# Performance work log

Measured on AMD Instinct MI355X. Metric: run time of the kernel, lower is better.

The kernel has to match this reference:

```python
import jax, jax.numpy as jnp
import numpy as np

B, S, D, H = 2, 2048, 2048, 16
HD = D // H
EPS = 1e-5


def layernorm(x, scale, shift):
    mean = jnp.mean(x, axis=-1, keepdims=True)
    var = jnp.mean((x - mean) ** 2, axis=-1, keepdims=True)  # unbiased=False
    return scale * (x - mean) / jnp.sqrt(var + EPS) + shift


def gelu_buggy(x):
    # Faithful to source: tanh is applied ONLY to the constant sqrt(2/pi)
    c = jnp.tanh(jnp.sqrt(jnp.asarray(2.0 / jnp.pi, dtype=x.dtype)))
    return 0.5 * x * (1.0 + c * (x + 0.044715 * x ** 3))


def setup_inputs() -> dict:
    key = jax.random.key(0)
    ks = jax.random.split(key, 10)
    sd = 0.02
    return {
        "x": jax.random.normal(ks[0], (B, S, D), dtype=jnp.float32),
        "wq": jax.random.normal(ks[1], (D, D), dtype=jnp.float32) * sd,
        "wk": jax.random.normal(ks[2], (D, D), dtype=jnp.float32) * sd,
        "wv": jax.random.normal(ks[3], (D, D), dtype=jnp.float32) * sd,
        "wo": jax.random.normal(ks[4], (D, D), dtype=jnp.float32) * sd,
        "bo": jnp.zeros((D,), dtype=jnp.float32),
        "w1": jax.random.normal(ks[5], (D, 4 * D), dtype=jnp.float32) * sd,
        "b1": jnp.zeros((4 * D,), dtype=jnp.float32),
        "w2": jax.random.normal(ks[6], (4 * D, D), dtype=jnp.float32) * sd,
        "b2": jnp.zeros((D,), dtype=jnp.float32),
        "ln_scale": jnp.ones((D,), dtype=jnp.float32),
        "ln_shift": jnp.zeros((D,), dtype=jnp.float32),
    }


def attention(h, wq, wk, wv, wo, bo):
    b, s, _ = h.shape
    q = (h @ wq).reshape(b, s, H, HD).transpose(0, 2, 1, 3)  # [b,h,s,hd]
    k = (h @ wk).reshape(b, s, H, HD).transpose(0, 2, 1, 3)
    v = (h @ wv).reshape(b, s, H, HD).transpose(0, 2, 1, 3)
    scores = jnp.einsum('bhqd,bhkd->bhqk', q, k)
    causal = jnp.tril(jnp.ones((s, s), dtype=bool))
    scores = jnp.where(causal, scores, -jnp.inf)
    w = jax.nn.softmax(scores / jnp.sqrt(jnp.asarray(HD, dtype=h.dtype)), axis=-1)
    ctx = jnp.einsum('bhqk,bhkd->bhqd', w, v).transpose(0, 2, 1, 3).reshape(b, s, D)
    return ctx @ wo + bo


def reference(x, wq, wk, wv, wo, bo, w1, b1, w2, b2, ln_scale, ln_shift):
    # NB: source applies ln1 before BOTH sub-blocks (ln2 unused); dropout is identity (p=0 / eval)
    shortcut = x
    h = layernorm(x, ln_scale, ln_shift)
    h = attention(h, wq, wk, wv, wo, bo)
    x = h + shortcut
    shortcut = x
    h = layernorm(x, ln_scale, ln_shift)
    h = gelu_buggy(h @ w1 + b1) @ w2 + b2
    return h + shortcut
```

## Files before the change

### kernel.cpp

```cpp
#include <hip/hip_runtime.h>
#include <hip/hip_bf16.h>
#include <math.h>


typedef short bf16x8 __attribute__((ext_vector_type(8)));
typedef float f32x4 __attribute__((ext_vector_type(4)));
typedef short short4v __attribute__((ext_vector_type(4)));

#define MFMA16x32(a, b, c) __builtin_amdgcn_mfma_f32_16x16x32_bf16((a), (b), (c), 0, 0, 0)

__device__ __forceinline__ short f2bs(float f) {
    unsigned u = __builtin_bit_cast(unsigned, f);
    unsigned r = (u + 0x7FFFu + ((u >> 16) & 1u)) >> 16;
    return (short)(unsigned short)r;
}

__device__ __forceinline__ void gload_lds16(const void* g, void* l) {
    __builtin_amdgcn_global_load_lds(
        (const __attribute__((address_space(1))) unsigned int*)g,
        (__attribute__((address_space(3))) unsigned int*)l, 16, 0, 0);
}

template <int N>
__device__ __forceinline__ void vmw() {
    if constexpr (N == 0) asm volatile("s_waitcnt vmcnt(0)" ::: "memory");
    else if constexpr (N == 6) asm volatile("s_waitcnt vmcnt(6)" ::: "memory");
    else if constexpr (N == 8) asm volatile("s_waitcnt vmcnt(8)" ::: "memory");
    else if constexpr (N == 12) asm volatile("s_waitcnt vmcnt(12)" ::: "memory");
}

__global__ __launch_bounds__(256) void transpose_kernel(const float* __restrict__ in,
                                                        short* __restrict__ out,
                                                        int R, int C) {
    __shared__ float tile[32][33];
    const int tx = threadIdx.x & 31;
    const int ty = threadIdx.x >> 5;
    const int c0 = blockIdx.x * 32;
    const int r0 = blockIdx.y * 32;
#pragma unroll
    for (int i = 0; i < 4; ++i) {
        int r = ty + i * 8;
        tile[r][tx] = in[(size_t)(r0 + r) * C + c0 + tx];
    }
    __syncthreads();
#pragma unroll
    for (int i = 0; i < 4; ++i) {
        int r = ty + i * 8;
        out[(size_t)(c0 + r) * R + r0 + tx] = f2bs(tile[tx][r]);
    }
}

__global__ __launch_bounds__(256) void ln_kernel(const float* __restrict__ x,
                                                 const float* __restrict__ sc,
                                                 const float* __restrict__ sh,
                                                 short* __restrict__ out) {
    const int D = 2048;
    const int row = blockIdx.x;
    const int tid = threadIdx.x;
    __shared__ float red[4];
    const float4* xr = (const float4*)(x + (size_t)row * D);
    float4 v0 = xr[tid];
    float4 v1 = xr[tid + 256];
    float vals0[4] = {v0.x, v0.y, v0.z, v0.w};
    float vals1[4] = {v1.x, v1.y, v1.z, v1.w};

    float s = vals0[0] + vals0[1] + vals0[2] + vals0[3] + vals1[0] + vals1[1] + vals1[2] + vals1[3];
#pragma unroll
    for (int off = 32; off; off >>= 1) s += __shfl_xor(s, off);
    if ((tid & 63) == 0) red[tid >> 6] = s;
    __syncthreads();
    float mean = (red[0] + red[1] + red[2] + red[3]) * (1.0f / 2048.0f);
    __syncthreads();

    float q = 0.0f;
#pragma unroll
    for (int j = 0; j < 4; ++j) {
        float t0 = vals0[j] - mean;
        float t1 = vals1[j] - mean;
        q += t0 * t0 + t1 * t1;
    }
#pragma unroll
    for (int off = 32; off; off >>= 1) q += __shfl_xor(q, off);
    if ((tid & 63) == 0) red[tid >> 6] = q;
    __syncthreads();
    float var = (red[0] + red[1] + red[2] + red[3]) * (1.0f / 2048.0f);
    float inv = rsqrtf(var + 1e-5f);

    const int c0 = tid * 4;
    const int c1 = (tid + 256) * 4;
    short4v o0, o1;
#pragma unroll
    for (int j = 0; j < 4; ++j) {
        o0[j] = f2bs(sc[c0 + j] * ((vals0[j] - mean) * inv) + sh[c0 + j]);
        o1[j] = f2bs(sc[c1 + j] * ((vals1[j] - mean) * inv) + sh[c1 + j]);
    }
    *(short4v*)(out + (size_t)row * D + c0) = o0;
    *(short4v*)(out + (size_t)row * D + c1) = o1;
}

template <int EPI>
__global__ __launch_bounds__(512, 2) void gemm256(const short* __restrict__ Aop,
                                                  const short* __restrict__ Bt,
                                                  int M, int N, int K,
                                                  void* __restrict__ Cout,
                                                  const float* __restrict__ bias,
                                                  const float* __restrict__ res,
                                                  float gconst) {
    constexpr int TSZ = 256 * 64;
    extern __shared__ __align__(16) short lds[];
    const int tid = threadIdx.x;
    const int lane = tid & 63;
    const int wid = tid >> 6;
    const int wm = wid >> 2, wn = wid & 3;
    const int l15 = lane & 15, grp = lane >> 4;

    const int gx = gridDim.x;
    int flat = (int)blockIdx.y * gx + (int)blockIdx.x;
    const int cpx = (gx * (int)gridDim.y) >> 3;
    flat = (flat & 7) * cpx + (flat >> 3);
    const int bx = flat % gx, by = flat / gx;
    const long m0 = (long)by * 256, n0 = (long)bx * 256;
    const int nt = K >> 6;

    f32x4 zero = {0.f, 0.f, 0.f, 0.f};
    f32x4 acc[8][4];
#pragma unroll
    for (int i = 0; i < 8; i++)
#pragma unroll
        for (int j = 0; j < 4; j++) acc[i][j] = zero;

    auto STAGE = [&](int t, short* bufA, short* bufB) {
        const long k0 = (long)t << 6;
#pragma unroll
        for (int j = 0; j < 4; ++j) {
            int c = tid + j * 512;
            int row = c >> 3, sl = (c & 7) ^ (row & 7);
            gload_lds16(Aop + (size_t)(m0 + row) * K + k0 + sl * 8, bufA + (size_t)c * 8);
        }
#pragma unroll
        for (int j = 0; j < 4; ++j) {
            int c = tid + j * 512;
            int row = c >> 3, sl = (c & 7) ^ (row & 7);
            gload_lds16(Bt + (size_t)(n0 + row) * K + k0 + sl * 8, bufB + (size_t)c * 8);
        }
    };

    STAGE(0, lds, lds + 2 * TSZ);
    STAGE(1, lds + TSZ, lds + 3 * TSZ);

    for (int t = 0; t < nt; ++t) {
        if (t == nt - 1) { vmw<0>(); } else { vmw<8>(); }
        __builtin_amdgcn_s_barrier();
        __builtin_amdgcn_sched_barrier(0);
        const short* bufA = lds + (t & 1) * TSZ;
        const short* bufB = lds + 2 * TSZ + (t & 1) * TSZ;
        __builtin_amdgcn_s_setprio(1);
#pragma unroll
        for (int kk = 0; kk < 2; ++kk) {
            bf16x8 af[8], bfr[4];
#pragma unroll
            for (int mi = 0; mi < 8; ++mi) {
                int row = wm * 128 + mi * 16 + l15;
                af[mi] = *(const bf16x8*)(bufA + row * 64 + (((kk * 4 + grp) ^ (row & 7)) * 8));
            }
#pragma unroll
            for (int ni = 0; ni < 4; ++ni) {
                int row = wn * 64 + ni * 16 + l15;
                bfr[ni] = *(const bf16x8*)(bufB + row * 64 + (((kk * 4 + grp) ^ (row & 7)) * 8));
            }
#pragma unroll
            for (int mi = 0; mi < 8; ++mi)
#pragma unroll
                for (int ni = 0; ni < 4; ++ni)
                    acc[mi][ni] = MFMA16x32(af[mi], bfr[ni], acc[mi][ni]);
        }
        __builtin_amdgcn_s_setprio(0);
        asm volatile("s_waitcnt lgkmcnt(0)" ::: "memory");
        __builtin_amdgcn_sched_barrier(0);
        __builtin_amdgcn_s_barrier();
        if (t + 2 < nt) STAGE(t + 2, lds + (t & 1) * TSZ, lds + 2 * TSZ + (t & 1) * TSZ);
    }

#pragma unroll
    for (int mi = 0; mi < 8; mi++) {
        long gr = m0 + wm * 128 + mi * 16 + grp * 4;
#pragma unroll
        for (int ni = 0; ni < 4; ni++) {
            long gcol = n0 + wn * 64 + ni * 16 + l15;
#pragma unroll
            for (int r = 0; r < 4; r++) {
                float vv = acc[mi][ni][r];
                long idx = (gr + r) * N + gcol;
                if constexpr (EPI == 0) {
                    ((short*)Cout)[idx] = f2bs(vv);
                } else if constexpr (EPI == 1) {
                    ((float*)Cout)[idx] = vv + bias[gcol] + res[idx];
                } else {
                    float tv = vv + bias[gcol];
                    float g = 0.5f * tv * (1.0f + gconst * (tv + 0.044715f * tv * tv * tv));
                    ((short*)Cout)[idx] = f2bs(g);
                }
            }
        }
    }
}

template <int EPI>
__global__ __launch_bounds__(512, 1) void gemm3d(const short* __restrict__ A,
                                                 const short* __restrict__ Bt,
                                                 int M, int N, int K,
                                                 void* __restrict__ Cout,
                                                 const float* __restrict__ bias,
                                                 const float* __restrict__ res,
                                                 float gconst) {
    extern __shared__ __align__(16) short lds[];
    const int tid = threadIdx.x;
    const int lane = tid & 63;
    const int wid = tid >> 6;
    const int wm = wid >> 1, wn = wid & 1;
    const int l15 = lane & 15, grp = lane >> 4;

    const int gx = gridDim.x;
    int flat = (int)blockIdx.y * gx + (int)blockIdx.x;
    const int cpx = (gx * (int)gridDim.y) >> 3;
    flat = (flat & 7) * cpx + (flat >> 3);
    const int bx = flat % gx, by = flat / gx;
    const long m0 = (long)by * 256, n0 = (long)bx * 128;

    f32x4 zero = {0.f, 0.f, 0.f, 0.f};
    f32x4 acc[4][4];
#pragma unroll
    for (int i = 0; i < 4; i++)
#pragma unroll
        for (int j = 0; j < 4; j++) acc[i][j] = zero;

    auto STAGE = [&](long k0, int b) {
        short* bufA = lds + b * 24576;
        short* bufB = bufA + 16384;
#pragma unroll
        for (int j = 0; j < 4; ++j) {
            int c = tid + j * 512;
            int row = c >> 3, sl = (c & 7) ^ (row & 7);
            gload_lds16(A + (size_t)(m0 + row) * K + k0 + sl * 8,
                        bufA + (size_t)(wid * 64 + j * 512) * 8);
        }
#pragma unroll
        for (int j = 0; j < 2; ++j) {
            int c = tid + j * 512;
            int row = c >> 3, sl = (c & 7) ^ (row & 7);
            gload_lds16(Bt + (size_t)(n0 + row) * K + k0 + sl * 8,
                        bufB + (size_t)(wid * 64 + j * 512) * 8);
        }
    };

    const int nt = K >> 6;
    STAGE(0, 0);
    STAGE(64, 1);
    int cur = 0, nx2 = 2;

    for (int t = 0; t < nt; ++t) {
        if (t + 2 < nt) {
            STAGE((long)(t + 2) * 64, nx2);
            vmw<12>();
        } else if (t + 1 < nt) {
            vmw<6>();
        } else {
            vmw<0>();
        }
        __builtin_amdgcn_s_barrier();
        __builtin_amdgcn_sched_barrier(0);

        const short* bufA = lds + cur * 24576;
        const short* bufB = bufA + 16384;
        bf16x8 af[2][4], bfr[2][4];
#pragma unroll
        for (int kk = 0; kk < 2; ++kk) {
#pragma unroll
            for (int m = 0; m < 4; ++m) {
                int row = wm * 64 + m * 16 + l15;
                af[kk][m] = *(const bf16x8*)(bufA + row * 64 + (((kk * 4 + grp) ^ (row & 7)) * 8));
            }
#pragma unroll
            for (int n = 0; n < 4; ++n) {
                int row = wn * 64 + n * 16 + l15;
                bfr[kk][n] = *(const bf16x8*)(bufB + row * 64 + (((kk * 4 + grp) ^ (row & 7)) * 8));
            }
        }
        __builtin_amdgcn_s_setprio(1);
#pragma unroll
        for (int kk = 0; kk < 2; ++kk)
#pragma unroll
            for (int m = 0; m < 4; ++m)
#pragma unroll
                for (int n = 0; n < 4; ++n)
                    acc[m][n] = MFMA16x32(af[kk][m], bfr[kk][n], acc[m][n]);
        __builtin_amdgcn_s_setprio(0);
        asm volatile("s_waitcnt lgkmcnt(0)" ::: "memory");
        __builtin_amdgcn_s_barrier();
        __builtin_amdgcn_sched_barrier(0);
        cur = (cur == 2) ? 0 : cur + 1;
        nx2 = (nx2 == 2) ? 0 : nx2 + 1;
    }

#pragma unroll
    for (int m = 0; m < 4; m++) {
        long gr = m0 + wm * 64 + m * 16 + grp * 4;
#pragma unroll
        for (int n = 0; n < 4; n++) {
            long gcol = n0 + wn * 64 + n * 16 + l15;
#pragma unroll
            for (int r = 0; r < 4; r++) {
                float vv = acc[m][n][r];
                long idx = (gr + r) * N + gcol;
                if (EPI == 0) {
                    ((short*)Cout)[idx] = f2bs(vv);
                } else if (EPI == 1) {
                    ((float*)Cout)[idx] = vv + bias[gcol] + res[idx];
                } else {
                    float t2 = vv + bias[gcol];
                    float g = 0.5f * t2 * (1.0f + gconst * (t2 + 0.044715f * t2 * t2 * t2));
                    ((short*)Cout)[idx] = f2bs(g);
                }
            }
        }
    }
}

__global__ __launch_bounds__(256) void reshape_v_kernel(const short* __restrict__ qkv,
                                                        short* __restrict__ Vt) {
    __shared__ short tile[32][33];
    const int bid = blockIdx.x;
    const int dt = bid & 3, st = (bid >> 2) & 63, bh = bid >> 8;
    const int b = bh >> 4, h = bh & 15;
    const int s0 = st * 32, d0 = dt * 32;
    const int tx = threadIdx.x & 31, ty = threadIdx.x >> 5;
#pragma unroll
    for (int i = 0; i < 4; ++i) {
        int s = ty + i * 8;
        tile[s][tx] = qkv[(size_t)(b * 2048 + s0 + s) * 6144 + 4096 + h * 128 + d0 + tx];
    }
    __syncthreads();
#pragma unroll
    for (int i = 0; i < 4; ++i) {
        int d = ty + i * 8;
        Vt[((size_t)bh * 128 + d0 + d) * 2048 + s0 + tx] = tile[tx][d];
    }
}

__global__ __launch_bounds__(256) void flash3_kernel(const short* __restrict__ qp,
                                                     const short* __restrict__ Vt,
                                                     short* __restrict__ ctx) {
    const int S = 2048, D = 2048, HD = 128, LD = 6144;
    __shared__ __align__(16) short Ks[2][64 * 128];
    __shared__ __align__(16) short Vs[2][64 * 128];
    __shared__ __align__(16) short Ps[4][16 * 64];
    const int tid = threadIdx.x;
    const int lane = tid & 63, wid = tid >> 6;
    const int l15 = lane & 15, grp = lane >> 4;

    int bid = (int)blockIdx.x;
    bid = (bid & 7) * 64 + (bid >> 3);
    const int p = bid & 15, bh = bid >> 4;
    const int b = bh >> 4, h = bh & 15;
    const int qtH = 31 - p;
    const int nH = qtH + 1;
    const float scale = 0.08838834764831845f;
    const float NEGINF = -__builtin_inff();

    const short* Kbase = qp + (size_t)b * S * LD + 2048 + (size_t)h * HD;
    const short* Vbase = Vt + (size_t)bh * 128 * S;
    short* Psw = &Ps[wid][0];

    f32x4 zero = {0.f, 0.f, 0.f, 0.f};
    bf16x8 aq[4];
    float m_[4], l_[4];
    f32x4 o[8];

    int qt = qtH;
    int qw = qt * 64 + wid * 16;
    {
        const short* qrow = qp + (size_t)(b * S + qw + l15) * LD + h * HD;
#pragma unroll
        for (int kc = 0; kc < 4; kc++) aq[kc] = *(const bf16x8*)(qrow + kc * 32 + grp * 8);
    }
#pragma unroll
    for (int r = 0; r < 4; r++) { m_[r] = NEGINF; l_[r] = 0.f; }
#pragma unroll
    for (int n = 0; n < 8; n++) o[n] = zero;

#pragma unroll
    for (int j = 0; j < 4; ++j) {
        int c = tid + j * 256;
        int r = c >> 4, sl = c & 15;
        gload_lds16(Kbase + (size_t)r * LD + ((sl ^ (r & 7)) * 8),
                    Ks[0] + (size_t)(wid * 64 + j * 256) * 8);
    }
#pragma unroll
    for (int j = 0; j < 4; ++j) {
        int c = tid + j * 256;
        int d = c >> 3, sl = c & 7;
        gload_lds16(Vbase + (size_t)d * S + ((sl ^ (d & 7)) * 8),
                    Vs[0] + (size_t)(wid * 64 + j * 256) * 8);
    }
    __syncthreads();

    int cur = 0;
    for (int i = 0; i < 33; ++i) {
        const int kt = (i < nH) ? i : (i - nH);
        const bool lastT = (kt == qt);

        if (i + 1 < 33) {
            const int ktn = (i + 1 < nH) ? (i + 1) : (i + 1 - nH);
            const long kn0 = (long)ktn * 64;
            const short* Kg = Kbase + (size_t)kn0 * LD;
            const short* Vg = Vbase + kn0;
            short* kd = Ks[cur ^ 1];
            short* vd = Vs[cur ^ 1];
#pragma unroll
            for (int j = 0; j < 4; ++j) {
                int c = tid + j * 256;
                int r = c >> 4, sl = c & 15;
                gload_lds16(Kg + (size_t)r * LD + ((sl ^ (r & 7)) * 8),
                            kd + (size_t)(wid * 64 + j * 256) * 8);
            }
#pragma unroll
            for (int j = 0; j < 4; ++j) {
                int c = tid + j * 256;
                int d = c >> 3, sl = c & 7;
                gload_lds16(Vg + (size_t)d * S + ((sl ^ (d & 7)) * 8),
                            vd + (size_t)(wid * 64 + j * 256) * 8);
            }
        }

        const short* Kc = Ks[cur];
        const short* Vc = Vs[cur];

        f32x4 s[4] = {zero, zero, zero, zero};
#pragma unroll
        for (int n = 0; n < 4; ++n) {
            int r = n * 16 + l15;
#pragma unroll
            for (int kc = 0; kc < 4; ++kc) {
                bf16x8 kb = *(const bf16x8*)(Kc + r * 128 + (((kc * 4 + grp) ^ (r & 7)) * 8));
                s[n] = MFMA16x32(aq[kc], kb, s[n]);
            }
        }

        float al[4];
#pragma unroll
        for (int r = 0; r < 4; ++r) {
            float v[4];
#pragma unroll
            for (int n = 0; n < 4; ++n) v[n] = s[n][r] * scale;
            if (lastT) {
                int qrel = wid * 16 + grp * 4 + r;
#pragma unroll
                for (int n = 0; n < 4; ++n)
                    if (n * 16 + l15 > qrel) v[n] = NEGINF;
            }
            float mx = fmaxf(fmaxf(v[0], v[1]), fmaxf(v[2], v[3]));
            mx = fmaxf(mx, __shfl_xor(mx, 1));
            mx = fmaxf(mx, __shfl_xor(mx, 2));
            mx = fmaxf(mx, __shfl_xor(mx, 4));
            mx = fmaxf(mx, __shfl_xor(mx, 8));
            float mn = fmaxf(m_[r], mx);
            float sc_ = __expf(m_[r] - mn);
            float rs = 0.f;
            int q = grp * 4 + r;
#pragma unroll
            for (int n = 0; n < 4; ++n) {
                v[n] = __expf(v[n] - mn);
                rs += v[n];
                Psw[q * 64 + (((n * 2 + (l15 >> 3)) ^ (q & 7)) * 8) + (l15 & 7)] = f2bs(v[n]);
            }
            rs += __shfl_xor(rs, 1);
            rs += __shfl_xor(rs, 2);
            rs += __shfl_xor(rs, 4);
            rs += __shfl_xor(rs, 8);
            l_[r] = l_[r] * sc_ + rs;
            m_[r] = mn;
            al[r] = sc_;
        }
#pragma unroll
        for (int n = 0; n < 8; n++) {
            f32x4 t = o[n];
            t[0] *= al[0]; t[1] *= al[1]; t[2] *= al[2]; t[3] *= al[3];
            o[n] = t;
        }

        bf16x8 pa[2];
#pragma unroll
        for (int kc = 0; kc < 2; ++kc)
            pa[kc] = *(const bf16x8*)(Psw + l15 * 64 + (((kc * 4 + grp) ^ (l15 & 7)) * 8));
#pragma unroll
        for (int n = 0; n < 8; ++n) {
            int d = n * 16 + l15;
#pragma unroll
            for (int kc = 0; kc < 2; ++kc) {
                bf16x8 vb = *(const bf16x8*)(Vc + d * 64 + (((kc * 4 + grp) ^ (d & 7)) * 8));
                o[n] = MFMA16x32(pa[kc], vb, o[n]);
            }
        }

        if (lastT) {
            float inv[4];
#pragma unroll
            for (int r = 0; r < 4; ++r) inv[r] = 1.0f / l_[r];
            short* cb_ = ctx + (size_t)(b * S + qw + grp * 4) * D + h * HD + l15;
#pragma unroll
            for (int n = 0; n < 8; ++n)
#pragma unroll
                for (int r = 0; r < 4; ++r)
                    cb_[(size_t)r * D + n * 16] = f2bs(o[n][r] * inv[r]);
            if (i < 32) {
                qt = 31 - qtH;
                qw = qt * 64 + wid * 16;
                const short* qrow = qp + (size_t)(b * S + qw + l15) * LD + h * HD;
#pragma unroll
                for (int kc = 0; kc < 4; kc++) aq[kc] = *(const bf16x8*)(qrow + kc * 32 + grp * 8);
#pragma unroll
                for (int r = 0; r < 4; r++) { m_[r] = NEGINF; l_[r] = 0.f; }
#pragma unroll
                for (int n = 0; n < 8; n++) o[n] = zero;
            }
        }
        __syncthreads();
        cur ^= 1;
    }
}

extern "C" void kernel_launch(void* const* d_in, const int* in_sizes, int n_in,
                              void* d_out, int out_size, void* d_ws, size_t ws_size,
                              hipStream_t stream) {
    const float* x    = (const float*)d_in[0];
    const float* wq   = (const float*)d_in[1];
    const float* wk   = (const float*)d_in[2];
    const float* wv   = (const float*)d_in[3];
    const float* wo   = (const float*)d_in[4];
    const float* bo   = (const float*)d_in[5];
    const float* w1   = (const float*)d_in[6];
    const float* b1   = (const float*)d_in[7];
    const float* w2   = (const float*)d_in[8];
    const float* b2   = (const float*)d_in[9];
    const float* lnsc = (const float*)d_in[10];
    const float* lnsh = (const float*)d_in[11];

    const int B = 2, S = 2048, D = 2048;
    const int M = B * S;
    const int LDS_256 = 4 * 256 * 64 * 2;
    const int LDS_3D  = 3 * 24576 * 2;

    char* p = (char*)d_ws;
    short* wqkvT = (short*)p; p += (size_t)3 * D * D * 2;
    short* woT   = (short*)p; p += (size_t)D * D * 2;
    short* w1T   = (short*)p; p += (size_t)4 * D * D * 2;
    short* w2T   = (short*)p; p += (size_t)4 * D * D * 2;
    short* lnb   = (short*)p; p += (size_t)M * D * 2;
    short* qkvb  = (short*)p;
    short* h1    = qkvb;
    p += (size_t)M * 3 * D * 2;
    short* ctxb  = (short*)p; p += (size_t)M * D * 2;
    float* x2    = (float*)p; p += (size_t)M * D * 4;

    short* Vt = (short*)x2;

    const float gconst = tanhf(sqrtf(2.0f / 3.14159265358979323846f));

    hipFuncSetAttribute((const void*)&gemm256<2>, hipFuncAttributeMaxDynamicSharedMemorySize, LDS_256);
    hipFuncSetAttribute((const void*)&gemm3d<0>, hipFuncAttributeMaxDynamicSharedMemorySize, LDS_3D);
    hipFuncSetAttribute((const void*)&gemm3d<1>, hipFuncAttributeMaxDynamicSharedMemorySize, LDS_3D);

    dim3 blk(256);
    transpose_kernel<<<dim3(64, 64), blk, 0, stream>>>(wq, wqkvT, D, D);
    transpose_kernel<<<dim3(64, 64), blk, 0, stream>>>(wk, wqkvT + (size_t)D * D, D, D);
    transpose_kernel<<<dim3(64, 64), blk, 0, stream>>>(wv, wqkvT + (size_t)2 * D * D, D, D);
    transpose_kernel<<<dim3(64, 64), blk, 0, stream>>>(wo, woT, D, D);
    transpose_kernel<<<dim3(256, 64), blk, 0, stream>>>(w1, w1T, D, 4 * D);
    transpose_kernel<<<dim3(64, 256), blk, 0, stream>>>(w2, w2T, 4 * D, D);

    ln_kernel<<<dim3(M), blk, 0, stream>>>(x, lnsc, lnsh, lnb);
    gemm3d<0><<<dim3(3 * D / 128, M / 256), dim3(512), LDS_3D, stream>>>(
        lnb, wqkvT, M, 3 * D, D, qkvb, nullptr, nullptr, 0.f);

    reshape_v_kernel<<<dim3(8192), blk, 0, stream>>>(qkvb, Vt);

    flash3_kernel<<<dim3(512), blk, 0, stream>>>(qkvb, Vt, ctxb);

    gemm3d<1><<<dim3(D / 128, M / 256), dim3(512), LDS_3D, stream>>>(
        ctxb, woT, M, D, D, x2, bo, x, 0.f);
    ln_kernel<<<dim3(M), blk, 0, stream>>>(x2, lnsc, lnsh, lnb);
    gemm256<2><<<dim3(4 * D / 256, M / 256), dim3(512), LDS_256, stream>>>(
        lnb, w1T, M, 4 * D, D, h1, b1, nullptr, gconst);
    gemm3d<1><<<dim3(D / 128, M / 256), dim3(512), LDS_3D, stream>>>(
        h1, w2T, M, D, 4 * D, (float*)d_out, b2, x2, 0.f);
}
```

Measured before the change: 627.5 us.

## Merge weight transposes, store residual in bf16, replace FFN1 GEMM with smaller-tile kernel

Folds the six weight transpose launches into one kernel that dispatches by block index. The intermediate residual x2 is now stored as bf16 instead of fp32, with a new bf16 layernorm and new GEMM epilogues that read and write it. The 256x256 FFN1 GEMM is replaced by a 256x128 tile kernel with a triple-buffered K=32 pipeline and higher occupancy. This cuts launch overhead and residual memory traffic, but rounding the residual to bf16 costs accuracy.

```diff
diff --git a/kernel.cpp b/kernel.cpp
--- a/kernel.cpp
+++ b/kernel.cpp
@@ -15,6 +15,11 @@
     return (short)(unsigned short)r;
 }
 
+__device__ __forceinline__ float bs2f(short s) {
+    unsigned u = ((unsigned)(unsigned short)s) << 16;
+    return __builtin_bit_cast(float, u);
+}
+
 __device__ __forceinline__ void gload_lds16(const void* g, void* l) {
     __builtin_amdgcn_global_load_lds(
         (const __attribute__((address_space(1))) unsigned int*)g,
@@ -24,19 +29,39 @@
 template <int N>
 __device__ __forceinline__ void vmw() {
     if constexpr (N == 0) asm volatile("s_waitcnt vmcnt(0)" ::: "memory");
+    else if constexpr (N == 3) asm volatile("s_waitcnt vmcnt(3)" ::: "memory");
     else if constexpr (N == 6) asm volatile("s_waitcnt vmcnt(6)" ::: "memory");
-    else if constexpr (N == 8) asm volatile("s_waitcnt vmcnt(8)" ::: "memory");
     else if constexpr (N == 12) asm volatile("s_waitcnt vmcnt(12)" ::: "memory");
 }
 
-__global__ __launch_bounds__(256) void transpose_kernel(const float* __restrict__ in,
-                                                        short* __restrict__ out,
-                                                        int R, int C) {
+__global__ __launch_bounds__(256) void transpose_all_kernel(
+    const float* __restrict__ wq, const float* __restrict__ wk,
+    const float* __restrict__ wv, const float* __restrict__ wo,
+    const float* __restrict__ w1, const float* __restrict__ w2,
+    short* __restrict__ wqkvT, short* __restrict__ woT,
+    short* __restrict__ w1T, short* __restrict__ w2T) {
+    const int D = 2048;
     __shared__ float tile[32][33];
+    int blk = blockIdx.x;
+    const float* in;
+    short* out;
+    int R, C, bx, by;
+    if (blk < 16384) {
+        int r = blk >> 12;
+        in = (r == 0) ? wq : (r == 1) ? wk : (r == 2) ? wv : wo;
+        out = (r < 3) ? (wqkvT + (size_t)r * D * D) : woT;
+        R = D; C = D;
+        int lb = blk & 4095; bx = lb & 63; by = lb >> 6;
+    } else if (blk < 32768) {
+        in = w1; out = w1T; R = D; C = 4 * D;
+        int lb = blk - 16384; bx = lb & 255; by = lb >> 8;
+    } else {
+        in = w2; out = w2T; R = 4 * D; C = D;
+        int lb = blk - 32768; bx = lb & 63; by = lb >> 6;
+    }
     const int tx = threadIdx.x & 31;
     const int ty = threadIdx.x >> 5;
-    const int c0 = blockIdx.x * 32;
-    const int r0 = blockIdx.y * 32;
+    const int c0 = bx * 32, r0 = by * 32;
 #pragma unroll
     for (int i = 0; i < 4; ++i) {
         int r = ty + i * 8;
@@ -98,111 +123,48 @@
     *(short4v*)(out + (size_t)row * D + c1) = o1;
 }
 
-template <int EPI>
-__global__ __launch_bounds__(512, 2) void gemm256(const short* __restrict__ Aop,
-                                                  const short* __restrict__ Bt,
-                                                  int M, int N, int K,
-                                                  void* __restrict__ Cout,
-                                                  const float* __restrict__ bias,
-                                                  const float* __restrict__ res,
-                                                  float gconst) {
-    constexpr int TSZ = 256 * 64;
-    extern __shared__ __align__(16) short lds[];
+__global__ __launch_bounds__(256) void ln_bf16_kernel(const short* __restrict__ x,
+                                                      const float* __restrict__ sc,
+                                                      const float* __restrict__ sh,
+                                                      short* __restrict__ out) {
+    const int D = 2048;
+    const int row = blockIdx.x;
     const int tid = threadIdx.x;
-    const int lane = tid & 63;
-    const int wid = tid >> 6;
-    const int wm = wid >> 2, wn = wid & 3;
-    const int l15 = lane & 15, grp = lane >> 4;
-
-    const int gx = gridDim.x;
-    int flat = (int)blockIdx.y * gx + (int)blockIdx.x;
-    const int cpx = (gx * (int)gridDim.y) >> 3;
-    flat = (flat & 7) * cpx + (flat >> 3);
-    const int bx = flat % gx, by = flat / gx;
-    const long m0 = (long)by * 256, n0 = (long)bx * 256;
-    const int nt = K >> 6;
-
-    f32x4 zero = {0.f, 0.f, 0.f, 0.f};
-    f32x4 acc[8][4];
-#pragma unroll
-    for (int i = 0; i < 8; i++)
-#pragma unroll
-        for (int j = 0; j < 4; j++) acc[i][j] = zero;
-
-    auto STAGE = [&](int t, short* bufA, short* bufB) {
-        const long k0 = (long)t << 6;
-#pragma unroll
-        for (int j = 0; j < 4; ++j) {
-            int c = tid + j * 512;
-            int row = c >> 3, sl = (c & 7) ^ (row & 7);
-            gload_lds16(Aop + (size_t)(m0 + row) * K + k0 + sl * 8, bufA + (size_t)c * 8);
-        }
-#pragma unroll
-        for (int j = 0; j < 4; ++j) {
-            int c = tid + j * 512;
-            int row = c >> 3, sl = (c & 7) ^ (row & 7);
-            gload_lds16(Bt + (size_t)(n0 + row) * K + k0 + sl * 8, bufB + (size_t)c * 8);
-        }
-    };
-
-    STAGE(0, lds, lds + 2 * TSZ);
-    STAGE(1, lds + TSZ, lds + 3 * TSZ);
-
-    for (int t = 0; t < nt; ++t) {
-        if (t == nt - 1) { vmw<0>(); } else { vmw<8>(); }
-        __builtin_amdgcn_s_barrier();
-        __builtin_amdgcn_sched_barrier(0);
-        const short* bufA = lds + (t & 1) * TSZ;
-        const short* bufB = lds + 2 * TSZ + (t & 1) * TSZ;
-        __builtin_amdgcn_s_setprio(1);
-#pragma unroll
-        for (int kk = 0; kk < 2; ++kk) {
-            bf16x8 af[8], bfr[4];
-#pragma unroll
-            for (int mi = 0; mi < 8; ++mi) {
-                int row = wm * 128 + mi * 16 + l15;
-                af[mi] = *(const bf16x8*)(bufA + row * 64 + (((kk * 4 + grp) ^ (row & 7)) * 8));
-            }
-#pragma unroll
-            for (int ni = 0; ni < 4; ++ni) {
-                int row = wn * 64 + ni * 16 + l15;
-                bfr[ni] = *(const bf16x8*)(bufB + row * 64 + (((kk * 4 + grp) ^ (row & 7)) * 8));
-            }
-#pragma unroll
-            for (int mi = 0; mi < 8; ++mi)
-#pragma unroll
-                for (int ni = 0; ni < 4; ++ni)
-                    acc[mi][ni] = MFMA16x32(af[mi], bfr[ni], acc[mi][ni]);
-        }
-        __builtin_amdgcn_s_setprio(0);
-        asm volatile("s_waitcnt lgkmcnt(0)" ::: "memory");
-        __builtin_amdgcn_sched_barrier(0);
-        __builtin_amdgcn_s_barrier();
-        if (t + 2 < nt) STAGE(t + 2, lds + (t & 1) * TSZ, lds + 2 * TSZ + (t & 1) * TSZ);
-    }
-
-#pragma unroll
-    for (int mi = 0; mi < 8; mi++) {
-        long gr = m0 + wm * 128 + mi * 16 + grp * 4;
-#pragma unroll
-        for (int ni = 0; ni < 4; ni++) {
-            long gcol = n0 + wn * 64 + ni * 16 + l15;
-#pragma unroll
-            for (int r = 0; r < 4; r++) {
-                float vv = acc[mi][ni][r];
-                long idx = (gr + r) * N + gcol;
-                if constexpr (EPI == 0) {
-                    ((short*)Cout)[idx] = f2bs(vv);
-                } else if constexpr (EPI == 1) {
-                    ((float*)Cout)[idx] = vv + bias[gcol] + res[idx];
-                } else {
-                    float tv = vv + bias[gcol];
-                    float g = 0.5f * tv * (1.0f + gconst * (tv + 0.044715f * tv * tv * tv));
-                    ((short*)Cout)[idx] = f2bs(g);
-                }
-            }
-        }
-    }
+    __shared__ float red[4];
+    bf16x8 v = *(const bf16x8*)(x + (size_t)row * D + tid * 8);
+    float vals[8];
+#pragma unroll
+    for (int j = 0; j < 8; ++j) vals[j] = bs2f(v[j]);
+
+    float s = 0.f;
+#pragma unroll
+    for (int j = 0; j < 8; ++j) s += vals[j];
+#pragma unroll
+    for (int off = 32; off; off >>= 1) s += __shfl_xor(s, off);
+    if ((tid & 63) == 0) red[tid >> 6] = s;
+    __syncthreads();
+    float mean = (red[0] + red[1] + red[2] + red[3]) * (1.0f / 2048.0f);
+    __syncthreads();
+
+    float q = 0.0f;
+#pragma unroll
+    for (int j = 0; j < 8; ++j) {
+        float t = vals[j] - mean;
+        q += t * t;
+    }
+#pragma unroll
+    for (int off = 32; off; off >>= 1) q += __shfl_xor(q, off);
+    if ((tid & 63) == 0) red[tid >> 6] = q;
+    __syncthreads();
+    float var = (red[0] + red[1] + red[2] + red[3]) * (1.0f / 2048.0f);
+    float inv = rsqrtf(var + 1e-5f);
+
+    const int c0 = tid * 8;
+    bf16x8 o;
+#pragma unroll
+    for (int j = 0; j < 8; ++j)
+        o[j] = f2bs(sc[c0 + j] * ((vals[j] - mean) * inv) + sh[c0 + j]);
+    *(bf16x8*)(out + (size_t)row * D + c0) = o;
 }
 
 template <int EPI>
@@ -312,14 +274,132 @@
             for (int r = 0; r < 4; r++) {
                 float vv = acc[m][n][r];
                 long idx = (gr + r) * N + gcol;
-                if (EPI == 0) {
+                if constexpr (EPI == 0) {
                     ((short*)Cout)[idx] = f2bs(vv);
-                } else if (EPI == 1) {
+                } else if constexpr (EPI == 1) {
                     ((float*)Cout)[idx] = vv + bias[gcol] + res[idx];
-                } else {
+                } else if constexpr (EPI == 2) {
                     float t2 = vv + bias[gcol];
                     float g = 0.5f * t2 * (1.0f + gconst * (t2 + 0.044715f * t2 * t2 * t2));
                     ((short*)Cout)[idx] = f2bs(g);
+                } else if constexpr (EPI == 3) {
+                    ((short*)Cout)[idx] = f2bs(vv + bias[gcol] + res[idx]);
+                } else {
+                    ((float*)Cout)[idx] = vv + bias[gcol] + bs2f(((const short*)res)[idx]);
+                }
+            }
+        }
+    }
+}
+
+template <int EPI>
+__global__ __launch_bounds__(512, 4) void gemm3b(const short* __restrict__ A,
+                                                 const short* __restrict__ Bt,
+                                                 int M, int N, int K,
+                                                 void* __restrict__ Cout,
+                                                 const float* __restrict__ bias,
+                                                 const float* __restrict__ res,
+                                                 float gconst) {
+    extern __shared__ __align__(16) short lds[];
+    const int tid = threadIdx.x;
+    const int lane = tid & 63;
+    const int wid = tid >> 6;
+    const int wm = wid >> 1, wn = wid & 1;
+    const int l15 = lane & 15, grp = lane >> 4;
+
+    const int gx = gridDim.x;
+    int flat = (int)blockIdx.y * gx + (int)blockIdx.x;
+    const int cpx = (gx * (int)gridDim.y) >> 3;
+    flat = (flat & 7) * cpx + (flat >> 3);
+    const int bx = flat % gx, by = flat / gx;
+    const long m0 = (long)by * 256, n0 = (long)bx * 128;
+
+    f32x4 zero = {0.f, 0.f, 0.f, 0.f};
+    f32x4 acc[4][4];
+#pragma unroll
+    for (int i = 0; i < 4; i++)
+#pragma unroll
+        for (int j = 0; j < 4; j++) acc[i][j] = zero;
+
+    auto STAGE = [&](int t, int b) {
+        short* bufA = lds + b * 12288;
+        short* bufB = bufA + 8192;
+        const long k0 = (long)t << 5;
+#pragma unroll
+        for (int j = 0; j < 2; ++j) {
+            int c = tid + j * 512;
+            int row = c >> 2, sl = (c & 3) ^ ((row ^ (row >> 2)) & 3);
+            gload_lds16(A + (size_t)(m0 + row) * K + k0 + sl * 8, bufA + (size_t)c * 8);
+        }
+        {
+            int c = tid;
+            int row = c >> 2, sl = (c & 3) ^ ((row ^ (row >> 2)) & 3);
+            gload_lds16(Bt + (size_t)(n0 + row) * K + k0 + sl * 8, bufB + (size_t)c * 8);
+        }
+    };
+
+    const int nt = K >> 5;
+    STAGE(0, 0);
+    STAGE(1, 1);
+    int cur = 0, nx2 = 2;
+
+    for (int t = 0; t < nt; ++t) {
+        if (t + 2 < nt) {
+            STAGE(t + 2, nx2);
+            vmw<6>();
+        } else if (t + 1 < nt) {
+            vmw<3>();
+        } else {
+            vmw<0>();
+        }
+        __builtin_amdgcn_s_barrier();
+        __builtin_amdgcn_sched_barrier(0);
+
+        const short* bufA = lds + cur * 12288;
+        const short* bufB = bufA + 8192;
+        bf16x8 af[4], bfr[4];
+#pragma unroll
+        for (int m = 0; m < 4; ++m) {
+            int row = wm * 64 + m * 16 + l15;
+            af[m] = *(const bf16x8*)(bufA + row * 32 + (((grp ^ (row ^ (row >> 2))) & 3) * 8));
+        }
+#pragma unroll
+        for (int n = 0; n < 4; ++n) {
+            int row = wn * 64 + n * 16 + l15;
+            bfr[n] = *(const bf16x8*)(bufB + row * 32 + (((grp ^ (row ^ (row >> 2))) & 3) * 8));
+        }
+        __builtin_amdgcn_s_setprio(1);
+#pragma unroll
+        for (int m = 0; m < 4; ++m)
+#pragma unroll
+            for (int n = 0; n < 4; ++n)
+                acc[m][n] = MFMA16x32(af[m], bfr[n], acc[m][n]);
+        __builtin_amdgcn_s_setprio(0);
+        asm volatile("s_waitcnt lgkmcnt(0)" ::: "memory");
+        __builtin_amdgcn_s_barrier();
+        __builtin_amdgcn_sched_barrier(0);
+        cur = (cur == 2) ? 0 : cur + 1;
+        nx2 = (nx2 == 2) ? 0 : nx2 + 1;
+    }
+
+#pragma unroll
+    for (int m = 0; m < 4; m++) {
+        long gr = m0 + wm * 64 + m * 16 + grp * 4;
+#pragma unroll
+        for (int n = 0; n < 4; n++) {
+            long gcol = n0 + wn * 64 + n * 16 + l15;
+#pragma unroll
+            for (int r = 0; r < 4; r++) {
+                float vv = acc[m][n][r];
+                long idx = (gr + r) * N + gcol;
+                if constexpr (EPI == 0) {
+                    ((short*)Cout)[idx] = f2bs(vv);
+                } else if constexpr (EPI == 2) {
+                    float t2 = vv + bias[gcol];
+                    float g = 0.5f * t2 * (1.0f + gconst * (t2 + 0.044715f * t2 * t2 * t2));
+                    ((short*)Cout)[idx] = f2bs(g);
+                } else {
+                    ((float*)Cout)[idx] = vv + bias[gcol] + res[idx];
                 }
             }
         }
@@ -547,8 +627,8 @@
 
     const int B = 2, S = 2048, D = 2048;
     const int M = B * S;
-    const int LDS_256 = 4 * 256 * 64 * 2;
-    const int LDS_3D  = 3 * 24576 * 2;
+    const int LDS_3D = 3 * 24576 * 2;
+    const int LDS_3B = 3 * 12288 * 2;
 
     char* p = (char*)d_ws;
     short* wqkvT = (short*)p; p += (size_t)3 * D * D * 2;
@@ -560,23 +640,20 @@
     short* h1    = qkvb;
     p += (size_t)M * 3 * D * 2;
     short* ctxb  = (short*)p; p += (size_t)M * D * 2;
-    float* x2    = (float*)p; p += (size_t)M * D * 4;
-
-    short* Vt = (short*)x2;
+    short* x2    = (short*)p; p += (size_t)M * D * 2;
+
+    short* Vt = x2;
 
     const float gconst = tanhf(sqrtf(2.0f / 3.14159265358979323846f));
 
-    hipFuncSetAttribute((const void*)&gemm256<2>, hipFuncAttributeMaxDynamicSharedMemorySize, LDS_256);
     hipFuncSetAttribute((const void*)&gemm3d<0>, hipFuncAttributeMaxDynamicSharedMemorySize, LDS_3D);
-    hipFuncSetAttribute((const void*)&gemm3d<1>, hipFuncAttributeMaxDynamicSharedMemorySize, LDS_3D);
+    hipFuncSetAttribute((const void*)&gemm3d<3>, hipFuncAttributeMaxDynamicSharedMemorySize, LDS_3D);
+    hipFuncSetAttribute((const void*)&gemm3d<4>, hipFuncAttributeMaxDynamicSharedMemorySize, LDS_3D);
+    hipFuncSetAttribute((const void*)&gemm3b<2>, hipFuncAttributeMaxDynamicSharedMemorySize, LDS_3B);
 
     dim3 blk(256);
-    transpose_kernel<<<dim3(64, 64), blk, 0, stream>>>(wq, wqkvT, D, D);
-    transpose_kernel<<<dim3(64, 64), blk, 0, stream>>>(wk, wqkvT + (size_t)D * D, D, D);
-    transpose_kernel<<<dim3(64, 64), blk, 0, stream>>>(wv, wqkvT + (size_t)2 * D * D, D, D);
-    transpose_kernel<<<dim3(64, 64), blk, 0, stream>>>(wo, woT, D, D);
-    transpose_kernel<<<dim3(256, 64), blk, 0, stream>>>(w1, w1T, D, 4 * D);
-    transpose_kernel<<<dim3(64, 256), blk, 0, stream>>>(w2, w2T, 4 * D, D);
+    transpose_all_kernel<<<dim3(49152), blk, 0, stream>>>(
+        wq, wk, wv, wo, w1, w2, wqkvT, woT, w1T, w2T);
 
     ln_kernel<<<dim3(M), blk, 0, stream>>>(x, lnsc, lnsh, lnb);
     gemm3d<0><<<dim3(3 * D / 128, M / 256), dim3(512), LDS_3D, stream>>>(
@@ -586,11 +663,11 @@
 
     flash3_kernel<<<dim3(512), blk, 0, stream>>>(qkvb, Vt, ctxb);
 
-    gemm3d<1><<<dim3(D / 128, M / 256), dim3(512), LDS_3D, stream>>>(
+    gemm3d<3><<<dim3(D / 128, M / 256), dim3(512), LDS_3D, stream>>>(
         ctxb, woT, M, D, D, x2, bo, x, 0.f);
-    ln_kernel<<<dim3(M), blk, 0, stream>>>(x2, lnsc, lnsh, lnb);
-    gemm256<2><<<dim3(4 * D / 256, M / 256), dim3(512), LDS_256, stream>>>(
+    ln_bf16_kernel<<<dim3(M), blk, 0, stream>>>(x2, lnsc, lnsh, lnb);
+    gemm3b<2><<<dim3(4 * D / 128, M / 256), dim3(512), LDS_3B, stream>>>(
         lnb, w1T, M, 4 * D, D, h1, b1, nullptr, gconst);
-    gemm3d<1><<<dim3(D / 128, M / 256), dim3(512), LDS_3D, stream>>>(
-        h1, w2T, M, D, 4 * D, (float*)d_out, b2, x2, 0.f);
-}
+    gemm3d<4><<<dim3(D / 128, M / 256), dim3(512), LDS_3D, stream>>>(
+        h1, w2T, M, D, 4 * D, (float*)d_out, b2, (const float*)x2, 0.f);
+}
```

After: 625.7 us. Within noise of the previous version (-0.3%).
